# Performance work log

Hardware: AMD Instinct MI355X
Metric: run time of the kernel (lower is better)

Reference implementation:

```python
import jax, jax.numpy as jnp
import numpy as np

N = 100000  # nodes
E = 600000  # edges
D = 128     # input_dim
H = D // 2  # hidden of MLP head
OUT = 10    # output_dim
EPS = 1e-5
NEG_SLOPE = 0.2


def _p(key, shape, scale):
    return jax.random.normal(key, shape, dtype=jnp.float32) * scale


def setup_inputs() -> dict:
    key = jax.random.key(0)
    ks = jax.random.split(key, 16)
    s = 1.0 / np.sqrt(D)
    return {
        "x": jax.random.normal(ks[0], (N, D), dtype=jnp.float32),
        "edge_index": jax.random.randint(ks[1], (2, E), 0, N, dtype=jnp.int64),
        # SAGEConv: lin_l (applied to mean-aggregated neighbors, has bias), lin_r (root)
        "sage_Wl": _p(ks[2], (D, D), s), "sage_Wr": _p(ks[3], (D, D), s),
        "sage_b": jnp.zeros((D,), jnp.float32),
        # GCNConv
        "gcn_W": _p(ks[4], (D, D), s), "gcn_b": jnp.zeros((D,), jnp.float32),
        # GATConv (heads=1)
        "gat_W": _p(ks[5], (D, D), s),
        "gat_att_src": _p(ks[6], (D,), s), "gat_att_dst": _p(ks[7], (D,), s),
        "gat_b": jnp.zeros((D,), jnp.float32),
        # BatchNorms (batch-stat normalization)
        "bn1_g": jnp.ones((D,), jnp.float32), "bn1_b": jnp.zeros((D,), jnp.float32),
        "bn2_g": jnp.ones((D,), jnp.float32), "bn2_b": jnp.zeros((D,), jnp.float32),
        "bn3_g": jnp.ones((D,), jnp.float32), "bn3_b": jnp.zeros((D,), jnp.float32),
        # MLP head
        "lin1_W": _p(ks[8], (D, H), s), "lin1_b": jnp.zeros((H,), jnp.float32),
        "lin2_W": _p(ks[9], (H, OUT), 1.0 / np.sqrt(H)), "lin2_b": jnp.zeros((OUT,), jnp.float32),
    }


def _bn_relu(x, g, b):
    mu = jnp.mean(x, axis=0)
    var = jnp.mean(jnp.square(x - mu), axis=0)
    return jax.nn.relu((x - mu) * jax.lax.rsqrt(var + EPS) * g + b)


def _sage(x, src, dst, Wl, Wr, b):
    agg = jax.ops.segment_sum(x[src], dst, num_segments=N)          # [N, D]
    cnt = jax.ops.segment_sum(jnp.ones((src.shape[0],), x.dtype), dst, num_segments=N)
    mean = agg / jnp.maximum(cnt, 1.0)[:, None]
    return mean @ Wl + x @ Wr + b


def _gcn(x, src, dst, W, b):
    loop = jnp.arange(N, dtype=src.dtype)
    s = jnp.concatenate([src, loop]); d = jnp.concatenate([dst, loop])
    deg = jax.ops.segment_sum(jnp.ones((d.shape[0],), x.dtype), d, num_segments=N)
    dinv = jnp.where(deg > 0, jax.lax.rsqrt(jnp.maximum(deg, 1.0)), 0.0)
    xw = x @ W
    msg = xw[s] * (dinv[s] * dinv[d])[:, None]
    return jax.ops.segment_sum(msg, d, num_segments=N) + b


def _gat(x, src, dst, W, att_s, att_d, b):
    loop = jnp.arange(N, dtype=src.dtype)
    s = jnp.concatenate([src, loop]); d = jnp.concatenate([dst, loop])
    xw = x @ W                                  # [N, D]
    a_s = xw @ att_s                            # [N]
    a_d = xw @ att_d                            # [N]
    e = jax.nn.leaky_relu(a_s[s] + a_d[d], NEG_SLOPE)  # [E+N]
    m = jax.ops.segment_max(e, d, num_segments=N)
    ee = jnp.exp(e - m[d])
    z = jax.ops.segment_sum(ee, d, num_segments=N)
    alpha = ee / z[d]
    return jax.ops.segment_sum(alpha[:, None] * xw[s], d, num_segments=N) + b


def reference(x, edge_index, sage_Wl, sage_Wr, sage_b, gcn_W, gcn_b,
              gat_W, gat_att_src, gat_att_dst, gat_b,
              bn1_g, bn1_b, bn2_g, bn2_b, bn3_g, bn3_b,
              lin1_W, lin1_b, lin2_W, lin2_b):
    src, dst = edge_index[0], edge_index[1]
    h = _bn_relu(_sage(x, src, dst, sage_Wl, sage_Wr, sage_b), bn1_g, bn1_b)
    h = _bn_relu(_gcn(h, src, dst, gcn_W, gcn_b), bn2_g, bn2_b)
    h = _bn_relu(_gat(h, src, dst, gat_W, gat_att_src, gat_att_dst, gat_b), bn3_g, bn3_b)
    # dropout is identity in eval mode
    h = jax.nn.relu(h @ lin1_W + lin1_b) @ lin2_W + lin2_b
    return jax.nn.log_softmax(h, axis=1)
```

## Files before the change

kernel.cpp:

```cpp
#include <hip/hip_runtime.h>

static constexpr int Dd = 128;
static constexpr int Hh = 64;
static constexpr int OC = 10;
#define CDIV(a,b) (((a)+(b)-1)/(b))

typedef __attribute__((ext_vector_type(8))) short short8v;
typedef __attribute__((ext_vector_type(16))) float f32x16;
typedef unsigned short u16;

__device__ __forceinline__ float lrelu(float x){ return x>0.f? x : 0.2f*x; }
__device__ __forceinline__ unsigned f2bf(float f){
  unsigned u = __float_as_uint(f);
  return (u + 0x7FFFu + ((u>>16)&1u)) >> 16;
}
__device__ __forceinline__ float bl(unsigned u){ return __uint_as_float(u<<16); }
__device__ __forceinline__ float bh(unsigned u){ return __uint_as_float(u & 0xFFFF0000u); }
__device__ __forceinline__ int swz(int byte, int row){ return byte ^ ((row&7)<<4); }

__global__ __launch_bounds__(256) void k_hist(const int* __restrict__ dst, int E,
    int* __restrict__ cnt) {
  int e = blockIdx.x*256 + threadIdx.x;
  if (e < E) atomicAdd(cnt + dst[e], 1);
}

__global__ __launch_bounds__(256) void k_scan_l1(const int* __restrict__ cnt,
    int* __restrict__ rp, int n, int* __restrict__ bsum) {
  __shared__ int sdata[256];
  int t = threadIdx.x;
  int base = blockIdx.x*2048 + t*8;
  int v[8]; int s = 0;
  #pragma unroll
  for (int k = 0; k < 8; k++) { v[k] = (base+k < n) ? cnt[base+k] : 0; s += v[k]; }
  sdata[t] = s; __syncthreads();
  for (int off = 1; off < 256; off <<= 1) {
    int a = sdata[t];
    int b = (t >= off) ? sdata[t-off] : 0;
    __syncthreads();
    sdata[t] = a + b;
    __syncthreads();
  }
  int ex = sdata[t] - s;
  if (t == 255) bsum[blockIdx.x] = sdata[255];
  int run = ex;
  #pragma unroll
  for (int k = 0; k < 8; k++) { if (base+k < n) rp[base+k] = run; run += v[k]; }
}

__global__ void k_scan_l2(int* __restrict__ bsum, int nb) {
  if (threadIdx.x == 0 && blockIdx.x == 0) {
    int run = 0;
    for (int i = 0; i < nb; i++) { int v = bsum[i]; bsum[i] = run; run += v; }
  }
}

__global__ __launch_bounds__(256) void k_scan_l3(int* __restrict__ rp, int n,
    const int* __restrict__ bsum, int E) {
  int off = bsum[blockIdx.x];
  int base = blockIdx.x*2048 + threadIdx.x*8;
  #pragma unroll
  for (int k = 0; k < 8; k++) if (base+k < n) rp[base+k] += off;
  if (blockIdx.x == 0 && threadIdx.x == 0) rp[n] = E;
}

__global__ __launch_bounds__(256) void k_fill(const int* __restrict__ src,
    const int* __restrict__ dst, int E, const int* __restrict__ rp,
    int* __restrict__ cnt, int* __restrict__ col) {
  int e = blockIdx.x*256 + threadIdx.x;
  if (e >= E) return;
  int d = dst[e];
  int pos = rp[d] + atomicSub(cnt + d, 1) - 1;
  col[pos] = src[e];
}

__global__ __launch_bounds__(256) void k_dinv(const int* __restrict__ rp,
    float* __restrict__ dinv, int n) {
  int i = blockIdx.x*256 + threadIdx.x;
  if (i < n) dinv[i] = rsqrtf((float)(rp[i+1] - rp[i]) + 1.0f);
}

__global__ __launch_bounds__(256) void k_wt_all(
    const float* __restrict__ w0, const float* __restrict__ w1,
    const float* __restrict__ w2, const float* __restrict__ w3,
    const float* __restrict__ w4,
    u16* __restrict__ o0, u16* __restrict__ o1, u16* __restrict__ o2,
    u16* __restrict__ o3, u16* __restrict__ o4) {
  int idx = blockIdx.x*256 + threadIdx.x;
  const float* W; u16* O; int base, N;
  if (idx < 65536) {
    int m = idx >> 14;
    W = m==0?w0 : m==1?w1 : m==2?w2 : w3;
    O = m==0?o0 : m==1?o1 : m==2?o2 : o3;
    base = idx & 16383; N = 128;
  } else if (idx < 73728) {
    W = w4; O = o4; base = idx - 65536; N = 64;
  } else return;
  int n = base / 128, k = base % 128;
  O[base] = (u16)f2bf(W[k*N + n]);
}

__global__ __launch_bounds__(256) void k_tobf16(const float* __restrict__ in,
    u16* __restrict__ out, int n8) {
  int idx = blockIdx.x*256 + threadIdx.x;
  if (idx >= n8) return;
  const float4* p = reinterpret_cast<const float4*>(in) + idx*2;
  float4 v0 = p[0], v1 = p[1];
  uint4 w;
  w.x = f2bf(v0.x) | (f2bf(v0.y)<<16);
  w.y = f2bf(v0.z) | (f2bf(v0.w)<<16);
  w.z = f2bf(v1.x) | (f2bf(v1.y)<<16);
  w.w = f2bf(v1.z) | (f2bf(v1.w)<<16);
  reinterpret_cast<uint4*>(out)[idx] = w;
}

__global__ __launch_bounds__(256) void k_sage_gather(const u16* __restrict__ xb,
    const int* __restrict__ rp, const int* __restrict__ col,
    u16* __restrict__ ob, int n) {
  int gid = blockIdx.x*256 + threadIdx.x;
  int i = gid >> 5, l = gid & 31;
  if (i >= n) return;
  int beg = rp[i], end = rp[i+1];
  const u16* xp = xb + l*4;
  float a0=0.f, a1=0.f, a2=0.f, a3=0.f;
  int j = beg;
  for (; j+4 <= end; j += 4) {
    int s0=col[j], s1=col[j+1], s2=col[j+2], s3=col[j+3];
    uint2 v0 = *reinterpret_cast<const uint2*>(xp + (size_t)s0*Dd);
    uint2 v1 = *reinterpret_cast<const uint2*>(xp + (size_t)s1*Dd);
    uint2 v2 = *reinterpret_cast<const uint2*>(xp + (size_t)s2*Dd);
    uint2 v3 = *reinterpret_cast<const uint2*>(xp + (size_t)s3*Dd);
    a0 += (bl(v0.x)+bl(v1.x)) + (bl(v2.x)+bl(v3.x));
    a1 += (bh(v0.x)+bh(v1.x)) + (bh(v2.x)+bh(v3.x));
    a2 += (bl(v0.y)+bl(v1.y)) + (bl(v2.y)+bl(v3.y));
    a3 += (bh(v0.y)+bh(v1.y)) + (bh(v2.y)+bh(v3.y));
  }
  for (; j < end; j++) {
    int s = col[j];
    uint2 v = *reinterpret_cast<const uint2*>(xp + (size_t)s*Dd);
    a0 += bl(v.x); a1 += bh(v.x); a2 += bl(v.y); a3 += bh(v.y);
  }
  float inv = 1.0f / fmaxf((float)(end - beg), 1.0f);
  uint2 o;
  o.x = f2bf(a0*inv) | (f2bf(a1*inv)<<16);
  o.y = f2bf(a2*inv) | (f2bf(a3*inv)<<16);
  *reinterpret_cast<uint2*>(ob + (size_t)i*Dd + l*4) = o;
}

__global__ __launch_bounds__(256) void k_gcn_gather(const u16* __restrict__ xb,
    const int* __restrict__ rp, const int* __restrict__ col,
    const float* __restrict__ dinv, u16* __restrict__ ob, int n) {
  int gid = blockIdx.x*256 + threadIdx.x;
  int i = gid >> 5, l = gid & 31;
  if (i >= n) return;
  int beg = rp[i], end = rp[i+1];
  const u16* xp = xb + l*4;
  float a0=0.f, a1=0.f, a2=0.f, a3=0.f;
  int j = beg;
  for (; j+4 <= end; j += 4) {
    int s0=col[j], s1=col[j+1], s2=col[j+2], s3=col[j+3];
    uint2 v0 = *reinterpret_cast<const uint2*>(xp + (size_t)s0*Dd);
    uint2 v1 = *reinterpret_cast<const uint2*>(xp + (size_t)s1*Dd);
    uint2 v2 = *reinterpret_cast<const uint2*>(xp + (size_t)s2*Dd);
    uint2 v3 = *reinterpret_cast<const uint2*>(xp + (size_t)s3*Dd);
    float w0 = dinv[s0], w1 = dinv[s1], w2 = dinv[s2], w3 = dinv[s3];
    a0 += (w0*bl(v0.x)+w1*bl(v1.x)) + (w2*bl(v2.x)+w3*bl(v3.x));
    a1 += (w0*bh(v0.x)+w1*bh(v1.x)) + (w2*bh(v2.x)+w3*bh(v3.x));
    a2 += (w0*bl(v0.y)+w1*bl(v1.y)) + (w2*bl(v2.y)+w3*bl(v3.y));
    a3 += (w0*bh(v0.y)+w1*bh(v1.y)) + (w2*bh(v2.y)+w3*bh(v3.y));
  }
  for (; j < end; j++) {
    int s = col[j];
    float w = dinv[s];
    uint2 v = *reinterpret_cast<const uint2*>(xp + (size_t)s*Dd);
    a0 += w*bl(v.x); a1 += w*bh(v.x); a2 += w*bl(v.y); a3 += w*bh(v.y);
  }
  float di = dinv[i];
  float ws = di*di;
  uint2 sv = *reinterpret_cast<const uint2*>(xp + (size_t)i*Dd);
  a0 = di*a0 + ws*bl(sv.x); a1 = di*a1 + ws*bh(sv.x);
  a2 = di*a2 + ws*bl(sv.y); a3 = di*a3 + ws*bh(sv.y);
  uint2 o;
  o.x = f2bf(a0) | (f2bf(a1)<<16);
  o.y = f2bf(a2) | (f2bf(a3)<<16);
  *reinterpret_cast<uint2*>(ob + (size_t)i*Dd + l*4) = o;
}

__global__ __launch_bounds__(256) void k_gat_gather(const u16* __restrict__ xb,
    const int* __restrict__ rp, const int* __restrict__ col,
    const float* __restrict__ a_s, const float* __restrict__ a_d,
    u16* __restrict__ ob, int n) {
  int gid = blockIdx.x*256 + threadIdx.x;
  int i = gid >> 5, l = gid & 31;
  if (i >= n) return;
  int beg = rp[i], end = rp[i+1];
  const u16* xp = xb + l*4;
  float ad = a_d[i];
  float m = lrelu(a_s[i] + ad);
  float z = 1.0f;
  uint2 sv = *reinterpret_cast<const uint2*>(xp + (size_t)i*Dd);
  float a0 = bl(sv.x), a1 = bh(sv.x), a2 = bl(sv.y), a3 = bh(sv.y);
  int j = beg;
  for (; j+4 <= end; j += 4) {
    int s0=col[j], s1=col[j+1], s2=col[j+2], s3=col[j+3];
    uint2 v0 = *reinterpret_cast<const uint2*>(xp + (size_t)s0*Dd);
    uint2 v1 = *reinterpret_cast<const uint2*>(xp + (size_t)s1*Dd);
    uint2 v2 = *reinterpret_cast<const uint2*>(xp + (size_t)s2*Dd);
    uint2 v3 = *reinterpret_cast<const uint2*>(xp + (size_t)s3*Dd);
    float e0 = lrelu(a_s[s0]+ad), e1 = lrelu(a_s[s1]+ad);
    float e2 = lrelu(a_s[s2]+ad), e3 = lrelu(a_s[s3]+ad);
    float mg = fmaxf(fmaxf(e0,e1), fmaxf(e2,e3));
    if (mg > m) {
      float r = __expf(m - mg);
      z *= r; a0 *= r; a1 *= r; a2 *= r; a3 *= r;
      m = mg;
    }
    float w0 = __expf(e0-m), w1 = __expf(e1-m);
    float w2 = __expf(e2-m), w3 = __expf(e3-m);
    z += (w0+w1) + (w2+w3);
    a0 += (w0*bl(v0.x)+w1*bl(v1.x)) + (w2*bl(v2.x)+w3*bl(v3.x));
    a1 += (w0*bh(v0.x)+w1*bh(v1.x)) + (w2*bh(v2.x)+w3*bh(v3.x));
    a2 += (w0*bl(v0.y)+w1*bl(v1.y)) + (w2*bl(v2.y)+w3*bl(v3.y));
    a3 += (w0*bh(v0.y)+w1*bh(v1.y)) + (w2*bh(v2.y)+w3*bh(v3.y));
  }
  for (; j < end; j++) {
    int s = col[j];
    uint2 v = *reinterpret_cast<const uint2*>(xp + (size_t)s*Dd);
    float e = lrelu(a_s[s]+ad);
    if (e > m) {
      float r = __expf(m - e);
      z *= r; a0 *= r; a1 *= r; a2 *= r; a3 *= r;
      m = e;
    }
    float w = __expf(e-m);
    z += w;
    a0 += w*bl(v.x); a1 += w*bh(v.x); a2 += w*bl(v.y); a3 += w*bh(v.y);
  }
  float inv = 1.0f / z;
  uint2 o;
  o.x = f2bf(a0*inv) | (f2bf(a1*inv)<<16);
  o.y = f2bf(a2*inv) | (f2bf(a3*inv)<<16);
  *reinterpret_cast<uint2*>(ob + (size_t)i*Dd + l*4) = o;
}

__global__ __launch_bounds__(256) void k_bn_stats_bf(const u16* __restrict__ X, int M,
    float* __restrict__ gsum, float* __restrict__ gsq) {
  __shared__ float ss[2][256];
  int t = threadIdx.x;
  int cd = t & 63;
  int rg = t >> 6;
  float s0=0.f, q0=0.f, s1=0.f, q1=0.f;
  const unsigned* Xu = reinterpret_cast<const unsigned*>(X);
  for (int r = blockIdx.x*4 + rg; r < M; r += gridDim.x*4) {
    unsigned v = Xu[(size_t)r*64 + cd];
    float a = bl(v), b = bh(v);
    s0 += a; q0 += a*a; s1 += b; q1 += b*b;
  }
  ss[0][t] = s0; ss[1][t] = q0; __syncthreads();
  float rs0 = 0.f, rq0 = 0.f;
  if (rg == 0) {
    rs0 = ss[0][cd] + ss[0][cd+64] + ss[0][cd+128] + ss[0][cd+192];
    rq0 = ss[1][cd] + ss[1][cd+64] + ss[1][cd+128] + ss[1][cd+192];
  }
  __syncthreads();
  ss[0][t] = s1; ss[1][t] = q1; __syncthreads();
  if (rg == 0) {
    float rs1 = ss[0][cd] + ss[0][cd+64] + ss[0][cd+128] + ss[0][cd+192];
    float rq1 = ss[1][cd] + ss[1][cd+64] + ss[1][cd+128] + ss[1][cd+192];
    atomicAdd(gsum + 2*cd,     rs0); atomicAdd(gsq + 2*cd,     rq0);
    atomicAdd(gsum + 2*cd + 1, rs1); atomicAdd(gsq + 2*cd + 1, rq1);
  }
}

template<int NCOLS, bool DUAL, bool BNA, bool STATS, bool BIASRELU, bool ATT, bool OUTBF>
__global__ __launch_bounds__(256) void k_mm(
    const u16* __restrict__ A1, const u16* __restrict__ A2,
    const u16* __restrict__ WT1, const u16* __restrict__ WT2,
    const float* __restrict__ bng, const float* __restrict__ bnb,
    const float* __restrict__ bsum_in, const float* __restrict__ bsq_in,
    const float* __restrict__ bias,
    void* __restrict__ Cout, int M,
    float* __restrict__ gsum, float* __restrict__ gsq,
    const float* __restrict__ att_sv, const float* __restrict__ att_dv,
    float* __restrict__ as_out, float* __restrict__ ad_out) {
  constexpr int NF = NCOLS/32;
  __shared__ char ldsA[128*128*2];
  __shared__ char ldsW[NCOLS*128*2];
  __shared__ float s_scale[128], s_shift[128];
  int t = threadIdx.x;
  int wave = t >> 6, l = t & 63;
  int lm = l & 31, h = l >> 5;
  int row0 = blockIdx.x*128;

  if constexpr (BNA) {
    if (t < 128) {
      float mu = bsum_in[t] / (float)M;
      float var = fmaxf(bsq_in[t] / (float)M - mu*mu, 0.f);
      float sc = bng[t] * rsqrtf(var + 1e-5f);
      s_scale[t] = sc;
      s_shift[t] = bnb[t] - mu*sc;
    }
    __syncthreads();
  }

  f32x16 acc[NF];
  #pragma unroll
  for (int nf = 0; nf < NF; nf++)
    #pragma unroll
    for (int i = 0; i < 16; i++) acc[nf][i] = 0.f;

  const int nph = DUAL ? 2 : 1;
  for (int ph = 0; ph < nph; ph++) {
    const u16* A = (DUAL && ph) ? A2 : A1;
    const u16* WT = (DUAL && ph) ? WT2 : WT1;
    #pragma unroll
    for (int i = 0; i < NCOLS*16/256; i++) {
      int c = i*256 + t; int nrow = c >> 4; int k0 = (c & 15) << 3;
      uint4 w = *reinterpret_cast<const uint4*>(WT + nrow*128 + k0);
      *reinterpret_cast<uint4*>(ldsW + swz(nrow*256 + k0*2, nrow)) = w;
    }
    #pragma unroll
    for (int i = 0; i < 8; i++) {
      int c = i*256 + t; int row = c >> 4; int k0 = (c & 15) << 3;
      uint4 w = {0,0,0,0};
      if (row0 + row < M)
        w = *reinterpret_cast<const uint4*>(A + (size_t)(row0+row)*128 + k0);
      if constexpr (BNA) {
        float4 sc0 = *reinterpret_cast<const float4*>(&s_scale[k0]);
        float4 sc1 = *reinterpret_cast<const float4*>(&s_scale[k0+4]);
        float4 sh0 = *reinterpret_cast<const float4*>(&s_shift[k0]);
        float4 sh1 = *reinterpret_cast<const float4*>(&s_shift[k0+4]);
        float e0 = fmaxf(bl(w.x)*sc0.x+sh0.x, 0.f), e1 = fmaxf(bh(w.x)*sc0.y+sh0.y, 0.f);
        float e2 = fmaxf(bl(w.y)*sc0.z+sh0.z, 0.f), e3 = fmaxf(bh(w.y)*sc0.w+sh0.w, 0.f);
        float e4 = fmaxf(bl(w.z)*sc1.x+sh1.x, 0.f), e5 = fmaxf(bh(w.z)*sc1.y+sh1.y, 0.f);
        float e6 = fmaxf(bl(w.w)*sc1.z+sh1.z, 0.f), e7 = fmaxf(bh(w.w)*sc1.w+sh1.w, 0.f);
        w.x = f2bf(e0) | (f2bf(e1)<<16);
        w.y = f2bf(e2) | (f2bf(e3)<<16);
        w.z = f2bf(e4) | (f2bf(e5)<<16);
        w.w = f2bf(e6) | (f2bf(e7)<<16);
      }
      *reinterpret_cast<uint4*>(ldsA + swz(row*256 + k0*2, row)) = w;
    }
    __syncthreads();
    #pragma unroll
    for (int ks = 0; ks < 8; ks++) {
      int kb = (ks*16 + h*8) * 2;
      int arow = wave*32 + lm;
      short8v af = *reinterpret_cast<short8v*>(ldsA + swz(arow*256 + kb, arow));
      #pragma unroll
      for (int nf = 0; nf < NF; nf++) {
        int brow = nf*32 + lm;
        short8v bf = *reinterpret_cast<short8v*>(ldsW + swz(brow*256 + kb, brow));
        acc[nf] = __builtin_amdgcn_mfma_f32_32x32x16_bf16(af, bf, acc[nf], 0, 0, 0);
      }
    }
    __syncthreads();
  }
  float* s_sum = reinterpret_cast<float*>(ldsW);
  float* s_sq  = s_sum + 128;
  if constexpr (STATS) {
    if (t < 128) { s_sum[t] = 0.f; s_sq[t] = 0.f; }
    __syncthreads();
  }
  #pragma unroll
  for (int nf = 0; nf < NF; nf++) {
    int colg = nf*32 + lm;
    float bv = 0.f;
    if constexpr (BIASRELU) bv = bias[colg];
    float ps = 0.f, pq = 0.f;
    #pragma unroll
    for (int reg = 0; reg < 16; reg++) {
      int row = row0 + wave*32 + (reg&3) + 8*(reg>>2) + 4*h;
      float v = acc[nf][reg];
      if constexpr (BIASRELU) v = fmaxf(v + bv, 0.f);
      if (row < M) {
        if constexpr (OUTBF)
          ((u16*)Cout)[(size_t)row*NCOLS + colg] = (u16)f2bf(v);
        else
          ((float*)Cout)[(size_t)row*NCOLS + colg] = v;
      }
      ps += v; pq += v*v;
    }
    if constexpr (STATS) {
      atomicAdd(&s_sum[colg], ps);
      atomicAdd(&s_sq[colg], pq);
    }
  }
  if constexpr (ATT) {
    float as_c[NF], ad_c[NF];
    #pragma unroll
    for (int nf = 0; nf < NF; nf++) { as_c[nf] = att_sv[nf*32+lm]; ad_c[nf] = att_dv[nf*32+lm]; }
    #pragma unroll
    for (int reg = 0; reg < 16; reg++) {
      float ps = 0.f, pd = 0.f;
      #pragma unroll
      for (int nf = 0; nf < NF; nf++) { float v = acc[nf][reg]; ps += v*as_c[nf]; pd += v*ad_c[nf]; }
      #pragma unroll
      for (int mm = 1; mm < 32; mm <<= 1) { ps += __shfl_xor(ps, mm); pd += __shfl_xor(pd, mm); }
      int row = row0 + wave*32 + (reg&3) + 8*(reg>>2) + 4*h;
      if (lm == 0 && row < M) { as_out[row] = ps; ad_out[row] = pd; }
    }
  }
  if constexpr (STATS) {
    __syncthreads();
    if (t < 128) { atomicAdd(gsum + t, s_sum[t]); atomicAdd(gsq + t, s_sq[t]); }
  }
}

__global__ __launch_bounds__(256) void k_head2(const float* __restrict__ M1,
    const float* __restrict__ W2, const float* __restrict__ b2,
    float* __restrict__ out, int n) {
  __shared__ float rows[256][65];
  __shared__ float w2s[Hh][OC];
  __shared__ float b2s[OC];
  int t = threadIdx.x;
  for (int i = t; i < Hh*OC; i += 256) w2s[i/OC][i%OC] = W2[i];
  if (t < OC) b2s[t] = b2[t];
  int r0 = blockIdx.x*256;
  #pragma unroll
  for (int i = 0; i < 16; i++) {
    int f = i*256 + t; int row = f >> 4; int c0 = (f & 15) << 2;
    float4 v = {0,0,0,0};
    if (r0 + row < n) v = *reinterpret_cast<const float4*>(M1 + (size_t)(r0+row)*Hh + c0);
    rows[row][c0+0] = v.x; rows[row][c0+1] = v.y;
    rows[row][c0+2] = v.z; rows[row][c0+3] = v.w;
  }
  __syncthreads();
  int row = r0 + t;
  if (row >= n) return;
  float p[OC];
  #pragma unroll
  for (int c = 0; c < OC; c++) p[c] = b2s[c];
  for (int k = 0; k < Hh; k++) {
    float a = rows[t][k];
    #pragma unroll
    for (int c = 0; c < OC; c++) p[c] += a * w2s[k][c];
  }
  float mx = p[0];
  #pragma unroll
  for (int c = 1; c < OC; c++) mx = fmaxf(mx, p[c]);
  float s = 0.f;
  #pragma unroll
  for (int c = 0; c < OC; c++) s += expf(p[c] - mx);
  float lse = mx + logf(s);
  #pragma unroll
  for (int c = 0; c < OC; c++) out[(size_t)row*OC + c] = p[c] - lse;
}

extern "C" void kernel_launch(void* const* d_in, const int* in_sizes, int n_in,
                              void* d_out, int out_size, void* d_ws, size_t ws_size,
                              hipStream_t stream) {
  const float* x       = (const float*)d_in[0];
  const int*   ei      = (const int*)d_in[1];
  const float* sage_Wl = (const float*)d_in[2];
  const float* sage_Wr = (const float*)d_in[3];
  const float* gcn_W   = (const float*)d_in[5];
  const float* gat_W   = (const float*)d_in[7];
  const float* att_s   = (const float*)d_in[8];
  const float* att_d   = (const float*)d_in[9];
  const float* bn1_g = (const float*)d_in[11], *bn1_b = (const float*)d_in[12];
  const float* bn2_g = (const float*)d_in[13], *bn2_b = (const float*)d_in[14];
  const float* bn3_g = (const float*)d_in[15], *bn3_b = (const float*)d_in[16];
  const float* lin1_W = (const float*)d_in[17], *lin1_b = (const float*)d_in[18];
  const float* lin2_W = (const float*)d_in[19], *lin2_b = (const float*)d_in[20];

  const int Nn = in_sizes[0] / Dd;
  const int Ee = in_sizes[1] / 2;
  const int* srcv = ei;
  const int* dstv = ei + Ee;

  u16* b0 = (u16*)d_ws;
  u16* b1 = b0 + (size_t)Nn*Dd;
  u16* b2 = b1 + (size_t)Nn*Dd;
  float* dinv  = (float*)(b2 + (size_t)Nn*Dd);
  float* a_s   = dinv + Nn;
  float* a_d   = a_s + Nn;
  float* bs    = a_d + Nn;
  float* bs1_sum = bs,        *bs1_sq = bs + 128;
  float* bs2_sum = bs + 256,  *bs2_sq = bs + 384;
  float* bs3_sum = bs + 512,  *bs3_sq = bs + 640;
  int* rp    = (int*)(bs + 768);
  int* cnt_i = rp + (Nn + 1);
  int* bsum  = cnt_i + Nn;
  int* col   = bsum + 64;
  u16* wt_sWl = (u16*)(col + Ee);
  u16* wt_sWr = wt_sWl + 128*128;
  u16* wt_gcn = wt_sWr + 128*128;
  u16* wt_gat = wt_gcn + 128*128;
  u16* wt_l1  = wt_gat + 128*128;

  const dim3 B(256);
  const dim3 Gn(CDIV(Nn, 256));
  const dim3 Gn32(CDIV(Nn*32, 256));
  const dim3 Ge(CDIV(Ee, 256));
  const dim3 Gmm(CDIV(Nn, 128));
  const dim3 Ghead(CDIV(Nn, 256));
  const dim3 Gstat(512);
  const int nscan = CDIV(Nn, 2048);

  hipMemsetAsync(cnt_i, 0, (size_t)Nn*sizeof(int), stream);
  hipMemsetAsync(bs, 0, 768*sizeof(float), stream);

  k_hist<<<Ge, B, 0, stream>>>(dstv, Ee, cnt_i);
  k_scan_l1<<<dim3(nscan), B, 0, stream>>>(cnt_i, rp, Nn, bsum);
  k_scan_l2<<<dim3(1), dim3(64), 0, stream>>>(bsum, nscan);
  k_scan_l3<<<dim3(nscan), B, 0, stream>>>(rp, Nn, bsum, Ee);
  k_fill<<<Ge, B, 0, stream>>>(srcv, dstv, Ee, rp, cnt_i, col);
  k_dinv<<<Gn, B, 0, stream>>>(rp, dinv, Nn);
  k_wt_all<<<dim3(288), B, 0, stream>>>(sage_Wl, sage_Wr, gcn_W, gat_W, lin1_W,
                                        wt_sWl, wt_sWr, wt_gcn, wt_gat, wt_l1);
  k_tobf16<<<dim3(CDIV(Nn*Dd/8, 256)), B, 0, stream>>>(x, b0, Nn*Dd/8);

  k_sage_gather<<<Gn32, B, 0, stream>>>(b0, rp, col, b1, Nn);
  k_mm<128, true, false, true, false, false, true><<<Gmm, B, 0, stream>>>(
      b1, b0, wt_sWl, wt_sWr, nullptr, nullptr, nullptr, nullptr, nullptr,
      b2, Nn, bs1_sum, bs1_sq, nullptr, nullptr, nullptr, nullptr);

  k_mm<128, false, true, false, false, false, true><<<Gmm, B, 0, stream>>>(
      b2, nullptr, wt_gcn, nullptr, bn1_g, bn1_b, bs1_sum, bs1_sq, nullptr,
      b0, Nn, nullptr, nullptr, nullptr, nullptr, nullptr, nullptr);
  k_gcn_gather<<<Gn32, B, 0, stream>>>(b0, rp, col, dinv, b1, Nn);
  k_bn_stats_bf<<<Gstat, B, 0, stream>>>(b1, Nn, bs2_sum, bs2_sq);

  k_mm<128, false, true, false, false, true, true><<<Gmm, B, 0, stream>>>(
      b1, nullptr, wt_gat, nullptr, bn2_g, bn2_b, bs2_sum, bs2_sq, nullptr,
      b2, Nn, nullptr, nullptr, att_s, att_d, a_s, a_d);
  k_gat_gather<<<Gn32, B, 0, stream>>>(b2, rp, col, a_s, a_d, b0, Nn);
  k_bn_stats_bf<<<Gstat, B, 0, stream>>>(b0, Nn, bs3_sum, bs3_sq);

  float* m1 = (float*)b1;
  k_mm<64, false, true, false, true, false, false><<<Gmm, B, 0, stream>>>(
      b0, nullptr, wt_l1, nullptr, bn3_g, bn3_b, bs3_sum, bs3_sq, lin1_b,
      m1, Nn, nullptr, nullptr, nullptr, nullptr, nullptr, nullptr);
  k_head2<<<Ghead, B, 0, stream>>>(m1, lin2_W, lin2_b, (float*)d_out, Nn);
}
```

Before: 400.5 us.

## Load GEMM A fragments directly to registers and pre-tile weights for conflict-free LDS

The matmul kernel stops staging the activation tile in LDS: each lane loads its own MFMA A-fragment rows straight from global memory into registers and applies the BN/ReLU transform there. The weight-transpose kernel now writes weights in a k-chunk-major tiled layout, so the LDS copy becomes a plain linear copy and B-fragment reads need no swizzle. This removes the A LDS round trip, halves LDS use (which may raise occupancy) and drops some barriers. In exchange, the per-lane global loads are strided 16-byte accesses across rows and may coalesce less well.

```diff
diff --git a/kernel.cpp b/kernel.cpp
--- a/kernel.cpp
+++ b/kernel.cpp
@@ -16,7 +16,6 @@
 }
 __device__ __forceinline__ float bl(unsigned u){ return __uint_as_float(u<<16); }
 __device__ __forceinline__ float bh(unsigned u){ return __uint_as_float(u & 0xFFFF0000u); }
-__device__ __forceinline__ int swz(int byte, int row){ return byte ^ ((row&7)<<4); }
 
 __global__ __launch_bounds__(256) void k_hist(const int* __restrict__ dst, int E,
     int* __restrict__ cnt) {
@@ -96,7 +95,8 @@
     W = w4; O = o4; base = idx - 65536; N = 64;
   } else return;
   int n = base / 128, k = base % 128;
-  O[base] = (u16)f2bf(W[k*N + n]);
+  int f = (k>>3)*N*8 + n*8 + (k&7);
+  O[f] = (u16)f2bf(W[k*N + n]);
 }
 
 __global__ __launch_bounds__(256) void k_tobf16(const float* __restrict__ in,
@@ -283,7 +283,6 @@
     const float* __restrict__ att_sv, const float* __restrict__ att_dv,
     float* __restrict__ as_out, float* __restrict__ ad_out) {
   constexpr int NF = NCOLS/32;
-  __shared__ char ldsA[128*128*2];
   __shared__ char ldsW[NCOLS*128*2];
   __shared__ float s_scale[128], s_shift[128];
   int t = threadIdx.x;
@@ -299,7 +298,6 @@
       s_scale[t] = sc;
       s_shift[t] = bnb[t] - mu*sc;
     }
-    __syncthreads();
   }
 
   f32x16 acc[NF];
@@ -307,28 +305,37 @@
   for (int nf = 0; nf < NF; nf++)
     #pragma unroll
     for (int i = 0; i < 16; i++) acc[nf][i] = 0.f;
+
+  const int arow = row0 + wave*32 + lm;
+  const bool rok = arow < M;
 
   const int nph = DUAL ? 2 : 1;
   for (int ph = 0; ph < nph; ph++) {
     const u16* A = (DUAL && ph) ? A2 : A1;
     const u16* WT = (DUAL && ph) ? WT2 : WT1;
+    uint4 araw[8];
+    const u16* ap = A + (size_t)arow*128 + h*8;
+    #pragma unroll
+    for (int ks = 0; ks < 8; ks++) {
+      araw[ks] = rok ? *reinterpret_cast<const uint4*>(ap + ks*16)
+                     : uint4{0,0,0,0};
+    }
     #pragma unroll
     for (int i = 0; i < NCOLS*16/256; i++) {
-      int c = i*256 + t; int nrow = c >> 4; int k0 = (c & 15) << 3;
-      uint4 w = *reinterpret_cast<const uint4*>(WT + nrow*128 + k0);
-      *reinterpret_cast<uint4*>(ldsW + swz(nrow*256 + k0*2, nrow)) = w;
-    }
-    #pragma unroll
-    for (int i = 0; i < 8; i++) {
-      int c = i*256 + t; int row = c >> 4; int k0 = (c & 15) << 3;
-      uint4 w = {0,0,0,0};
-      if (row0 + row < M)
-        w = *reinterpret_cast<const uint4*>(A + (size_t)(row0+row)*128 + k0);
+      int c = i*256 + t;
+      reinterpret_cast<uint4*>(ldsW)[c] = reinterpret_cast<const uint4*>(WT)[c];
+    }
+    __syncthreads();
+    short8v af[8];
+    #pragma unroll
+    for (int ks = 0; ks < 8; ks++) {
+      uint4 w = araw[ks];
       if constexpr (BNA) {
-        float4 sc0 = *reinterpret_cast<const float4*>(&s_scale[k0]);
-        float4 sc1 = *reinterpret_cast<const float4*>(&s_scale[k0+4]);
-        float4 sh0 = *reinterpret_cast<const float4*>(&s_shift[k0]);
-        float4 sh1 = *reinterpret_cast<const float4*>(&s_shift[k0+4]);
+        int kbase = ks*16 + h*8;
+        float4 sc0 = *reinterpret_cast<const float4*>(&s_scale[kbase]);
+        float4 sc1 = *reinterpret_cast<const float4*>(&s_scale[kbase+4]);
+        float4 sh0 = *reinterpret_cast<const float4*>(&s_shift[kbase]);
+        float4 sh1 = *reinterpret_cast<const float4*>(&s_shift[kbase+4]);
         float e0 = fmaxf(bl(w.x)*sc0.x+sh0.x, 0.f), e1 = fmaxf(bh(w.x)*sc0.y+sh0.y, 0.f);
         float e2 = fmaxf(bl(w.y)*sc0.z+sh0.z, 0.f), e3 = fmaxf(bh(w.y)*sc0.w+sh0.w, 0.f);
         float e4 = fmaxf(bl(w.z)*sc1.x+sh1.x, 0.f), e5 = fmaxf(bh(w.z)*sc1.y+sh1.y, 0.f);
@@ -338,26 +345,23 @@
         w.z = f2bf(e4) | (f2bf(e5)<<16);
         w.w = f2bf(e6) | (f2bf(e7)<<16);
       }
-      *reinterpret_cast<uint4*>(ldsA + swz(row*256 + k0*2, row)) = w;
-    }
-    __syncthreads();
+      af[ks] = *reinterpret_cast<short8v*>(&w);
+    }
     #pragma unroll
     for (int ks = 0; ks < 8; ks++) {
-      int kb = (ks*16 + h*8) * 2;
-      int arow = wave*32 + lm;
-      short8v af = *reinterpret_cast<short8v*>(ldsA + swz(arow*256 + kb, arow));
+      int kc = ks*2 + h;
       #pragma unroll
       for (int nf = 0; nf < NF; nf++) {
-        int brow = nf*32 + lm;
-        short8v bf = *reinterpret_cast<short8v*>(ldsW + swz(brow*256 + kb, brow));
-        acc[nf] = __builtin_amdgcn_mfma_f32_32x32x16_bf16(af, bf, acc[nf], 0, 0, 0);
+        short8v bf = *reinterpret_cast<short8v*>(ldsW + (kc*NCOLS + nf*32 + lm)*16);
+        acc[nf] = __builtin_amdgcn_mfma_f32_32x32x16_bf16(af[ks], bf, acc[nf], 0, 0, 0);
       }
     }
-    __syncthreads();
+    if (DUAL && ph == 0) __syncthreads();
   }
   float* s_sum = reinterpret_cast<float*>(ldsW);
   float* s_sq  = s_sum + 128;
   if constexpr (STATS) {
+    __syncthreads();
     if (t < 128) { s_sum[t] = 0.f; s_sq[t] = 0.f; }
     __syncthreads();
   }
```

New measurement: 401.8 us. Within noise of the previous version (+0.3%).

## Fuse MLP head into lin1 GEMM and pre-layout weights for MFMA fragments

Applied to the files above, without the earlier changes.

Fuses the second linear layer and log-softmax into the lin1 matmul epilogue, so the intermediate fp32 hidden matrix is no longer written to and reread from global memory and one launch is removed. Weights are transposed once into an MFMA-fragment-ordered layout so the B tile is copied into LDS linearly and read with contiguous fragment loads, without swizzling. The A tile swaps XOR swizzling for a padded 272-byte row stride, and the per-phase barrier is rearranged. The head epilogue stages activations in LDS and uses only half the threads for the small GEMV, and the padding raises LDS use.

```diff
diff --git a/kernel.cpp b/kernel.cpp
--- a/kernel.cpp
+++ b/kernel.cpp
@@ -16,7 +16,6 @@
 }
 __device__ __forceinline__ float bl(unsigned u){ return __uint_as_float(u<<16); }
 __device__ __forceinline__ float bh(unsigned u){ return __uint_as_float(u & 0xFFFF0000u); }
-__device__ __forceinline__ int swz(int byte, int row){ return byte ^ ((row&7)<<4); }
 
 __global__ __launch_bounds__(256) void k_hist(const int* __restrict__ dst, int E,
     int* __restrict__ cnt) {
@@ -96,7 +95,9 @@
     W = w4; O = o4; base = idx - 65536; N = 64;
   } else return;
   int n = base / 128, k = base % 128;
-  O[base] = (u16)f2bf(W[k*N + n]);
+  int kc = k >> 3, nf = n >> 5, lm = n & 31;
+  int fi = (((kc*(N>>5) + nf)*32 + lm) << 3) | (k & 7);
+  O[fi] = (u16)f2bf(W[k*N + n]);
 }
 
 __global__ __launch_bounds__(256) void k_tobf16(const float* __restrict__ in,
@@ -271,7 +272,7 @@
   }
 }
 
-template<int NCOLS, bool DUAL, bool BNA, bool STATS, bool BIASRELU, bool ATT, bool OUTBF>
+template<int NCOLS, bool DUAL, bool BNA, bool STATS, bool BIASRELU, bool ATT, bool OUTBF, bool HEAD>
 __global__ __launch_bounds__(256) void k_mm(
     const u16* __restrict__ A1, const u16* __restrict__ A2,
     const u16* __restrict__ WT1, const u16* __restrict__ WT2,
@@ -281,11 +282,15 @@
     void* __restrict__ Cout, int M,
     float* __restrict__ gsum, float* __restrict__ gsq,
     const float* __restrict__ att_sv, const float* __restrict__ att_dv,
-    float* __restrict__ as_out, float* __restrict__ ad_out) {
+    float* __restrict__ as_out, float* __restrict__ ad_out,
+    const float* __restrict__ W2, const float* __restrict__ b2) {
   constexpr int NF = NCOLS/32;
-  __shared__ char ldsA[128*128*2];
-  __shared__ char ldsW[NCOLS*128*2];
+  __shared__ char ldsA[128*272];
+  __shared__ char ldsW[NCOLS*256];
   __shared__ float s_scale[128], s_shift[128];
+  __shared__ float s_sum[128], s_sq[128];
+  __shared__ float w2s[Hh][OC];
+  __shared__ float b2s[OC];
   int t = threadIdx.x;
   int wave = t >> 6, l = t & 63;
   int lm = l & 31, h = l >> 5;
@@ -299,8 +304,15 @@
       s_scale[t] = sc;
       s_shift[t] = bnb[t] - mu*sc;
     }
-    __syncthreads();
-  }
+  }
+  if constexpr (STATS) {
+    if (t < 128) { s_sum[t] = 0.f; s_sq[t] = 0.f; }
+  }
+  if constexpr (HEAD) {
+    for (int i = t; i < Hh*OC; i += 256) w2s[i/OC][i%OC] = W2[i];
+    if (t < OC) b2s[t] = b2[t];
+  }
+  if (BNA || STATS || HEAD) __syncthreads();
 
   f32x16 acc[NF];
   #pragma unroll
@@ -310,14 +322,9 @@
 
   const int nph = DUAL ? 2 : 1;
   for (int ph = 0; ph < nph; ph++) {
+    if (ph) __syncthreads();
     const u16* A = (DUAL && ph) ? A2 : A1;
     const u16* WT = (DUAL && ph) ? WT2 : WT1;
-    #pragma unroll
-    for (int i = 0; i < NCOLS*16/256; i++) {
-      int c = i*256 + t; int nrow = c >> 4; int k0 = (c & 15) << 3;
-      uint4 w = *reinterpret_cast<const uint4*>(WT + nrow*128 + k0);
-      *reinterpret_cast<uint4*>(ldsW + swz(nrow*256 + k0*2, nrow)) = w;
-    }
     #pragma unroll
     for (int i = 0; i < 8; i++) {
       int c = i*256 + t; int row = c >> 4; int k0 = (c & 15) << 3;
@@ -338,28 +345,64 @@
         w.z = f2bf(e4) | (f2bf(e5)<<16);
         w.w = f2bf(e6) | (f2bf(e7)<<16);
       }
-      *reinterpret_cast<uint4*>(ldsA + swz(row*256 + k0*2, row)) = w;
+      *reinterpret_cast<uint4*>(ldsA + row*272 + k0*2) = w;
+    }
+    #pragma unroll
+    for (int i = 0; i < NCOLS/16; i++) {
+      int c = i*256 + t;
+      reinterpret_cast<uint4*>(ldsW)[c] = reinterpret_cast<const uint4*>(WT)[c];
     }
     __syncthreads();
     #pragma unroll
     for (int ks = 0; ks < 8; ks++) {
-      int kb = (ks*16 + h*8) * 2;
+      int kc = ks*2 + h;
       int arow = wave*32 + lm;
-      short8v af = *reinterpret_cast<short8v*>(ldsA + swz(arow*256 + kb, arow));
+      short8v af = *reinterpret_cast<short8v*>(ldsA + arow*272 + kc*16);
       #pragma unroll
       for (int nf = 0; nf < NF; nf++) {
-        int brow = nf*32 + lm;
-        short8v bf = *reinterpret_cast<short8v*>(ldsW + swz(brow*256 + kb, brow));
+        short8v bf = *reinterpret_cast<short8v*>(ldsW + ((kc*NF + nf)*32 + lm)*16);
         acc[nf] = __builtin_amdgcn_mfma_f32_32x32x16_bf16(af, bf, acc[nf], 0, 0, 0);
       }
     }
+  }
+  if constexpr (HEAD) {
     __syncthreads();
-  }
-  float* s_sum = reinterpret_cast<float*>(ldsW);
-  float* s_sq  = s_sum + 128;
-  if constexpr (STATS) {
-    if (t < 128) { s_sum[t] = 0.f; s_sq[t] = 0.f; }
+    float* mrow = reinterpret_cast<float*>(ldsA);
+    #pragma unroll
+    for (int nf = 0; nf < NF; nf++) {
+      int colg = nf*32 + lm;
+      float bv = bias[colg];
+      #pragma unroll
+      for (int reg = 0; reg < 16; reg++) {
+        int row = wave*32 + (reg&3) + 8*(reg>>2) + 4*h;
+        mrow[row*65 + colg] = fmaxf(acc[nf][reg] + bv, 0.f);
+      }
+    }
     __syncthreads();
+    if (t < 128) {
+      int row = row0 + t;
+      if (row < M) {
+        float p[OC];
+        #pragma unroll
+        for (int c = 0; c < OC; c++) p[c] = b2s[c];
+        for (int k = 0; k < Hh; k++) {
+          float a = mrow[t*65 + k];
+          #pragma unroll
+          for (int c = 0; c < OC; c++) p[c] += a * w2s[k][c];
+        }
+        float mx = p[0];
+        #pragma unroll
+        for (int c = 1; c < OC; c++) mx = fmaxf(mx, p[c]);
+        float s = 0.f;
+        #pragma unroll
+        for (int c = 0; c < OC; c++) s += __expf(p[c] - mx);
+        float lse = mx + __logf(s);
+        #pragma unroll
+        for (int c = 0; c < OC; c++)
+          ((float*)Cout)[(size_t)row*OC + c] = p[c] - lse;
+      }
+    }
+    return;
   }
   #pragma unroll
   for (int nf = 0; nf < NF; nf++) {
@@ -404,46 +447,6 @@
     __syncthreads();
     if (t < 128) { atomicAdd(gsum + t, s_sum[t]); atomicAdd(gsq + t, s_sq[t]); }
   }
-}
-
-__global__ __launch_bounds__(256) void k_head2(const float* __restrict__ M1,
-    const float* __restrict__ W2, const float* __restrict__ b2,
-    float* __restrict__ out, int n) {
-  __shared__ float rows[256][65];
-  __shared__ float w2s[Hh][OC];
-  __shared__ float b2s[OC];
-  int t = threadIdx.x;
-  for (int i = t; i < Hh*OC; i += 256) w2s[i/OC][i%OC] = W2[i];
-  if (t < OC) b2s[t] = b2[t];
-  int r0 = blockIdx.x*256;
-  #pragma unroll
-  for (int i = 0; i < 16; i++) {
-    int f = i*256 + t; int row = f >> 4; int c0 = (f & 15) << 2;
-    float4 v = {0,0,0,0};
-    if (r0 + row < n) v = *reinterpret_cast<const float4*>(M1 + (size_t)(r0+row)*Hh + c0);
-    rows[row][c0+0] = v.x; rows[row][c0+1] = v.y;
-    rows[row][c0+2] = v.z; rows[row][c0+3] = v.w;
-  }
-  __syncthreads();
-  int row = r0 + t;
-  if (row >= n) return;
-  float p[OC];
-  #pragma unroll
-  for (int c = 0; c < OC; c++) p[c] = b2s[c];
-  for (int k = 0; k < Hh; k++) {
-    float a = rows[t][k];
-    #pragma unroll
-    for (int c = 0; c < OC; c++) p[c] += a * w2s[k][c];
-  }
-  float mx = p[0];
-  #pragma unroll
-  for (int c = 1; c < OC; c++) mx = fmaxf(mx, p[c]);
-  float s = 0.f;
-  #pragma unroll
-  for (int c = 0; c < OC; c++) s += expf(p[c] - mx);
-  float lse = mx + logf(s);
-  #pragma unroll
-  for (int c = 0; c < OC; c++) out[(size_t)row*OC + c] = p[c] - lse;
 }
 
 extern "C" void kernel_launch(void* const* d_in, const int* in_sizes, int n_in,
@@ -493,7 +496,6 @@
   const dim3 Gn32(CDIV(Nn*32, 256));
   const dim3 Ge(CDIV(Ee, 256));
   const dim3 Gmm(CDIV(Nn, 128));
-  const dim3 Ghead(CDIV(Nn, 256));
   const dim3 Gstat(512);
   const int nscan = CDIV(Nn, 2048);
 
@@ -511,25 +513,24 @@
   k_tobf16<<<dim3(CDIV(Nn*Dd/8, 256)), B, 0, stream>>>(x, b0, Nn*Dd/8);
 
   k_sage_gather<<<Gn32, B, 0, stream>>>(b0, rp, col, b1, Nn);
-  k_mm<128, true, false, true, false, false, true><<<Gmm, B, 0, stream>>>(
+  k_mm<128, true, false, true, false, false, true, false><<<Gmm, B, 0, stream>>>(
       b1, b0, wt_sWl, wt_sWr, nullptr, nullptr, nullptr, nullptr, nullptr,
-      b2, Nn, bs1_sum, bs1_sq, nullptr, nullptr, nullptr, nullptr);
-
-  k_mm<128, false, true, false, false, false, true><<<Gmm, B, 0, stream>>>(
+      b2, Nn, bs1_sum, bs1_sq, nullptr, nullptr, nullptr, nullptr, nullptr, nullptr);
+
+  k_mm<128, false, true, false, false, false, true, false><<<Gmm, B, 0, stream>>>(
       b2, nullptr, wt_gcn, nullptr, bn1_g, bn1_b, bs1_sum, bs1_sq, nullptr,
-      b0, Nn, nullptr, nullptr, nullptr, nullptr, nullptr, nullptr);
+      b0, Nn, nullptr, nullptr, nullptr, nullptr, nullptr, nullptr, nullptr, nullptr);
   k_gcn_gather<<<Gn32, B, 0, stream>>>(b0, rp, col, dinv, b1, Nn);
   k_bn_stats_bf<<<Gstat, B, 0, stream>>>(b1, Nn, bs2_sum, bs2_sq);
 
-  k_mm<128, false, true, false, false, true, true><<<Gmm, B, 0, stream>>>(
+  k_mm<128, false, true, false, false, true, true, false><<<Gmm, B, 0, stream>>>(
       b1, nullptr, wt_gat, nullptr, bn2_g, bn2_b, bs2_sum, bs2_sq, nullptr,
-      b2, Nn, nullptr, nullptr, att_s, att_d, a_s, a_d);
+      b2, Nn, nullptr, nullptr, att_s, att_d, a_s, a_d, nullptr, nullptr);
   k_gat_gather<<<Gn32, B, 0, stream>>>(b2, rp, col, a_s, a_d, b0, Nn);
   k_bn_stats_bf<<<Gstat, B, 0, stream>>>(b0, Nn, bs3_sum, bs3_sq);
 
-  float* m1 = (float*)b1;
-  k_mm<64, false, true, false, true, false, false><<<Gmm, B, 0, stream>>>(
+  k_mm<64, false, true, false, true, false, false, true><<<Gmm, B, 0, stream>>>(
       b0, nullptr, wt_l1, nullptr, bn3_g, bn3_b, bs3_sum, bs3_sq, lin1_b,
-      m1, Nn, nullptr, nullptr, nullptr, nullptr, nullptr, nullptr);
-  k_head2<<<Ghead, B, 0, stream>>>(m1, lin2_W, lin2_b, (float*)d_out, Nn);
-}
+      (float*)d_out, Nn, nullptr, nullptr, nullptr, nullptr, nullptr, nullptr,
+      lin2_W, lin2_b);
+}
```

Result: faster. 381.9 us (-4.6%).
